# Kernel optimization log

Measured on AMD Instinct MI355X. Metric: run time of the kernel, lower is better.

Reference implementation:

```python
import jax, jax.numpy as jnp
import numpy as np

N_NODES = 100000
N_EDGES = 1600000
IN_C, HID_C, OUT_C = 128, 256, 256


def sage_conv(x, src, dst, W_l, b_l, W_r, n_nodes):
    # mean aggregation of source-node features onto destination nodes
    msg_sum = jax.ops.segment_sum(x[src], dst, num_segments=n_nodes)  # [N, F]
    deg = jax.ops.segment_sum(jnp.ones_like(dst, dtype=x.dtype), dst, num_segments=n_nodes)
    aggr = msg_sum / jnp.maximum(deg, 1.0)[:, None]
    # PyG SAGEConv: lin_l(aggr) (with bias) + lin_r(x) (no bias)
    return aggr @ W_l + b_l + x @ W_r


def setup_inputs() -> dict:
    key = jax.random.key(0)
    ks = jax.random.split(key, 12)
    x = jax.random.normal(ks[0], (N_NODES, IN_C), dtype=jnp.float32)
    edge_src = jax.random.randint(ks[1], (N_EDGES,), 0, N_NODES)
    edge_dst = jax.random.randint(ks[2], (N_EDGES,), 0, N_NODES)

    def glorot(k, fan_in, fan_out):
        s = jnp.sqrt(2.0 / (fan_in + fan_out)).astype(jnp.float32)
        return jax.random.normal(k, (fan_in, fan_out), dtype=jnp.float32) * s

    return {
        "x": x,
        "W_l0": glorot(ks[3], IN_C, HID_C), "b_l0": jnp.zeros((HID_C,), jnp.float32),
        "W_r0": glorot(ks[4], IN_C, HID_C),
        "W_l1": glorot(ks[5], HID_C, HID_C), "b_l1": jnp.zeros((HID_C,), jnp.float32),
        "W_r1": glorot(ks[6], HID_C, HID_C),
        "W_l2": glorot(ks[7], HID_C, OUT_C), "b_l2": jnp.zeros((OUT_C,), jnp.float32),
        "W_r2": glorot(ks[8], HID_C, OUT_C),
        "edge_src": edge_src,
        "edge_dst": edge_dst,
    }


def reference(x, W_l0, b_l0, W_r0, W_l1, b_l1, W_r1, W_l2, b_l2, W_r2, edge_src, edge_dst):
    n = x.shape[0]
    h = sage_conv(x, edge_src, edge_dst, W_l0, b_l0, W_r0, n)
    h = jax.nn.relu(h)  # dropout p=0.0 -> identity
    h = sage_conv(h, edge_src, edge_dst, W_l1, b_l1, W_r1, n)
    h = jax.nn.relu(h)
    h = sage_conv(h, edge_src, edge_dst, W_l2, b_l2, W_r2, n)
    return h
```

## Files before the change

kernel.cpp:

```cpp
#include <hip/hip_runtime.h>
#include <cstdint>
#include <cstddef>


#define N_NODES 100000
#define N_EDGES 1600000

#define SCAN_BLOCKS 256
#define SCAN_T 256
#define FILL_PASSES 4

typedef unsigned short ushort;
typedef unsigned int uint;
typedef __attribute__((ext_vector_type(8))) short short8;
typedef __attribute__((ext_vector_type(4))) float floatx4;

#define AS1 __attribute__((address_space(1)))
#define AS3 __attribute__((address_space(3)))

__device__ __forceinline__ float bf2f(ushort h) {
    union { uint u; float f; } c; c.u = ((uint)h) << 16; return c.f;
}
__device__ __forceinline__ ushort f2bf(float f) {
    union { float f; uint u; } c; c.f = f;
    uint u = c.u;
    return (ushort)((u + 0x7FFFu + ((u >> 16) & 1u)) >> 16);
}


#define N4X (N_NODES * 128 / 4)

__global__ void prep_all(
    const int* __restrict__ dst, int* __restrict__ cnt,
    const float* __restrict__ x, ushort* __restrict__ xb,
    const float* __restrict__ Wl0, ushort* __restrict__ Wl0t,
    const float* __restrict__ Wr0, ushort* __restrict__ Wr0t,
    const float* __restrict__ Wl1, ushort* __restrict__ Wl1t,
    const float* __restrict__ Wr1, ushort* __restrict__ Wr1t,
    const float* __restrict__ Wl2, ushort* __restrict__ Wl2t,
    const float* __restrict__ Wr2, ushort* __restrict__ Wr2t)
{
    int i = blockIdx.x * blockDim.x + threadIdx.x;
    if (i < N_EDGES) { atomicAdd(&cnt[dst[i]], 1); return; }
    i -= N_EDGES;
    if (i < N4X) {
        float4 v = *(const float4*)&x[(size_t)i * 4];
        ushort4 o;
        o.x = f2bf(v.x); o.y = f2bf(v.y); o.z = f2bf(v.z); o.w = f2bf(v.w);
        *(ushort4*)&xb[(size_t)i * 4] = o;
        return;
    }
    i -= N4X;
    if (i < 32768) { Wl0t[i] = f2bf(Wl0[(i & 127) * 256 + (i >> 7)]); return; }
    i -= 32768;
    if (i < 32768) { Wr0t[i] = f2bf(Wr0[(i & 127) * 256 + (i >> 7)]); return; }
    i -= 32768;
    if (i < 65536) { Wl1t[i] = f2bf(Wl1[(i & 255) * 256 + (i >> 8)]); return; }
    i -= 65536;
    if (i < 65536) { Wr1t[i] = f2bf(Wr1[(i & 255) * 256 + (i >> 8)]); return; }
    i -= 65536;
    if (i < 65536) { Wl2t[i] = f2bf(Wl2[(i & 255) * 256 + (i >> 8)]); return; }
    i -= 65536;
    if (i < 65536) { Wr2t[i] = f2bf(Wr2[(i & 255) * 256 + (i >> 8)]); return; }
}


__global__ __launch_bounds__(SCAN_T) void scan_partial(
    const int* __restrict__ cnt, int* __restrict__ bsum, int n)
{
    int chunk = (n + SCAN_BLOCKS - 1) / SCAN_BLOCKS;
    int beg = blockIdx.x * chunk;
    int end = beg + chunk; if (end > n) end = n;
    int t = threadIdx.x;
    int s = 0;
    for (int i = beg + t; i < end; i += SCAN_T) s += cnt[i];
    __shared__ int sh[SCAN_T];
    sh[t] = s;
    __syncthreads();
    for (int off = SCAN_T / 2; off > 0; off >>= 1) {
        if (t < off) sh[t] += sh[t + off];
        __syncthreads();
    }
    if (t == 0) bsum[blockIdx.x] = sh[0];
}

__global__ __launch_bounds__(SCAN_T) void scan_block_sums(int* __restrict__ bsum) {
    int t = threadIdx.x;
    __shared__ int sh[SCAN_T];
    int v = bsum[t];
    sh[t] = v;
    __syncthreads();
    for (int off = 1; off < SCAN_T; off <<= 1) {
        int u = (t >= off) ? sh[t - off] : 0;
        __syncthreads();
        sh[t] += u;
        __syncthreads();
    }
    bsum[t] = sh[t] - v;
}

__global__ __launch_bounds__(SCAN_T) void scan_fill(
    int* __restrict__ cnt, const int* __restrict__ bsum,
    int* __restrict__ row_ptr, int n)
{
    int chunk = (n + SCAN_BLOCKS - 1) / SCAN_BLOCKS;
    int beg = blockIdx.x * chunk;
    int end = beg + chunk; if (end > n) end = n;
    int t = threadIdx.x;
    int per = (chunk + SCAN_T - 1) / SCAN_T;
    int tb = beg + t * per;
    int te = tb + per; if (te > end) te = end;
    int s = 0;
    for (int i = tb; i < te; ++i) s += cnt[i];
    __shared__ int sh[SCAN_T];
    sh[t] = s;
    __syncthreads();
    for (int off = 1; off < SCAN_T; off <<= 1) {
        int u = (t >= off) ? sh[t - off] : 0;
        __syncthreads();
        sh[t] += u;
        __syncthreads();
    }
    int running = bsum[blockIdx.x] + sh[t] - s;
    for (int i = tb; i < te; ++i) {
        int c = cnt[i];
        row_ptr[i] = running;
        cnt[i] = running;
        running += c;
    }
    if (blockIdx.x == 0 && t == 0) row_ptr[n] = N_EDGES;
}

__global__ void fill_csr(const int* __restrict__ src, const int* __restrict__ dst,
                         int* __restrict__ cursor, int* __restrict__ col_idx) {
    int i = blockIdx.x * blockDim.x + threadIdx.x;
    if (i >= N_EDGES) return;
    int lo = (int)blockIdx.y * (N_NODES / FILL_PASSES);
    int hi = lo + (N_NODES / FILL_PASSES);
    int d = dst[i];
    if (d >= lo && d < hi) {
        int p = atomicAdd(&cursor[d], 1);
        col_idx[p] = src[i];
    }
}

__global__ __launch_bounds__(64) void aggregate_bf16(
    const ushort* __restrict__ xb, const int* __restrict__ row_ptr,
    const int* __restrict__ col_idx, ushort* __restrict__ outb, int F)
{
    int node = blockIdx.x;
    int lane = threadIdx.x;
    int half = lane >> 5, li = lane & 31;
    int b = row_ptr[node], e = row_ptr[node + 1];
    float d = (float)(e - b); if (d < 1.f) d = 1.f;
    float inv = 1.f / d;

    if (F == 256) {
        float a[8];
#pragma unroll
        for (int j = 0; j < 8; ++j) a[j] = 0.f;
        const int c = li * 8;
        int i = b;
        for (; i + 7 < e; i += 8) {
            int s0 = col_idx[i + half];
            int s1 = col_idx[i + 2 + half];
            int s2 = col_idx[i + 4 + half];
            int s3 = col_idx[i + 6 + half];
            uint4 v0 = *(const uint4*)&xb[(size_t)s0 * 256 + c];
            uint4 v1 = *(const uint4*)&xb[(size_t)s1 * 256 + c];
            uint4 v2 = *(const uint4*)&xb[(size_t)s2 * 256 + c];
            uint4 v3 = *(const uint4*)&xb[(size_t)s3 * 256 + c];
#define ACC4(v) \
            a[0] += bf2f((ushort)(v.x & 0xffff)); a[1] += bf2f((ushort)(v.x >> 16)); \
            a[2] += bf2f((ushort)(v.y & 0xffff)); a[3] += bf2f((ushort)(v.y >> 16)); \
            a[4] += bf2f((ushort)(v.z & 0xffff)); a[5] += bf2f((ushort)(v.z >> 16)); \
            a[6] += bf2f((ushort)(v.w & 0xffff)); a[7] += bf2f((ushort)(v.w >> 16));
            ACC4(v0) ACC4(v1) ACC4(v2) ACC4(v3)
        }
        for (; i + 1 < e; i += 2) {
            int s0 = col_idx[i + half];
            uint4 v0 = *(const uint4*)&xb[(size_t)s0 * 256 + c];
            ACC4(v0)
        }
        if (i < e && half == 0) {
            int s0 = col_idx[i];
            uint4 v0 = *(const uint4*)&xb[(size_t)s0 * 256 + c];
            ACC4(v0)
        }
#undef ACC4
#pragma unroll
        for (int j = 0; j < 8; ++j) a[j] += __shfl(a[j], li + 32);
        if (half == 0) {
            short8 o;
#pragma unroll
            for (int j = 0; j < 8; ++j) o[j] = (short)f2bf(a[j] * inv);
            *(short8*)&outb[(size_t)node * 256 + c] = o;
        }
    } else {
        float a[4];
#pragma unroll
        for (int j = 0; j < 4; ++j) a[j] = 0.f;
        const int c = li * 4;
        int i = b;
        for (; i + 7 < e; i += 8) {
            int s0 = col_idx[i + half];
            int s1 = col_idx[i + 2 + half];
            int s2 = col_idx[i + 4 + half];
            int s3 = col_idx[i + 6 + half];
            uint2 v0 = *(const uint2*)&xb[(size_t)s0 * 128 + c];
            uint2 v1 = *(const uint2*)&xb[(size_t)s1 * 128 + c];
            uint2 v2 = *(const uint2*)&xb[(size_t)s2 * 128 + c];
            uint2 v3 = *(const uint2*)&xb[(size_t)s3 * 128 + c];
#define ACC2(v) \
            a[0] += bf2f((ushort)(v.x & 0xffff)); a[1] += bf2f((ushort)(v.x >> 16)); \
            a[2] += bf2f((ushort)(v.y & 0xffff)); a[3] += bf2f((ushort)(v.y >> 16));
            ACC2(v0) ACC2(v1) ACC2(v2) ACC2(v3)
        }
        for (; i + 1 < e; i += 2) {
            int s0 = col_idx[i + half];
            uint2 v0 = *(const uint2*)&xb[(size_t)s0 * 128 + c];
            ACC2(v0)
        }
        if (i < e && half == 0) {
            int s0 = col_idx[i];
            uint2 v0 = *(const uint2*)&xb[(size_t)s0 * 128 + c];
            ACC2(v0)
        }
#undef ACC2
#pragma unroll
        for (int j = 0; j < 4; ++j) a[j] += __shfl(a[j], li + 32);
        if (half == 0) {
            ushort4 o;
            o.x = f2bf(a[0] * inv); o.y = f2bf(a[1] * inv);
            o.z = f2bf(a[2] * inv); o.w = f2bf(a[3] * inv);
            *(ushort4*)&outb[(size_t)node * 128 + c] = o;
        }
    }
}

__global__ __launch_bounds__(512, 1) void gemm_wres(
    const ushort* __restrict__ A1, const ushort* __restrict__ W1t,
    const ushort* __restrict__ A2, const ushort* __restrict__ W2t,
    const float* __restrict__ bias, ushort* __restrict__ out_bf,
    float* __restrict__ out_f32, int M, int K, int relu)
{
    __shared__ __align__(16) ushort Wl[32 * 256 * 8];
    int tid = threadIdx.x;
    int w = tid >> 6, lane = tid & 63;
    int m_ = lane & 15, koq = lane >> 4;
    int row0 = blockIdx.x * 256;
    int KQ = K >> 3;
    int nj = (KQ * 256) >> 9;
    int nk = K >> 5;

    floatx4 acc[2][16];
#pragma unroll
    for (int i = 0; i < 2; ++i)
#pragma unroll
        for (int f = 0; f < 16; ++f) acc[i][f] = (floatx4){0.f, 0.f, 0.f, 0.f};

    int ra = row0 + w * 32 + m_;      if (ra > M - 1) ra = M - 1;
    int rb = row0 + w * 32 + 16 + m_; if (rb > M - 1) rb = M - 1;

    for (int mm = 0; mm < 2; ++mm) {
        const ushort* __restrict__ A  = mm ? A2 : A1;
        const ushort* __restrict__ Wt = mm ? W2t : W1t;
        if (mm) __syncthreads();
        for (int j = 0; j < nj; ++j) {
            int s = j * 512 + tid;
            int q = s >> 8, col = s & 255;
            __builtin_amdgcn_global_load_lds(
                (const AS1 uint*)&Wt[(size_t)col * K + q * 8],
                (AS3 uint*)&Wl[(size_t)(j * 512 + w * 64) * 8], 16, 0, 0);
        }
        __syncthreads();

        const ushort* __restrict__ Aa = &A[(size_t)ra * K + koq * 8];
        const ushort* __restrict__ Ab = &A[(size_t)rb * K + koq * 8];

        short8 a0 = *(const short8*)&Aa[0];
        short8 a1 = *(const short8*)&Ab[0];
        for (int kk = 0; kk < nk; ++kk) {
            short8 n0, n1;
            if (kk + 1 < nk) {
                n0 = *(const short8*)&Aa[(kk + 1) * 32];
                n1 = *(const short8*)&Ab[(kk + 1) * 32];
            }
            const ushort* bbase = &Wl[(size_t)((kk * 4 + koq) * 256 + m_) * 8];
#pragma unroll
            for (int fc = 0; fc < 16; ++fc) {
                short8 b = *(const short8*)&bbase[fc * 128];
                acc[0][fc] = __builtin_amdgcn_mfma_f32_16x16x32_bf16(a0, b, acc[0][fc], 0, 0, 0);
                acc[1][fc] = __builtin_amdgcn_mfma_f32_16x16x32_bf16(a1, b, acc[1][fc], 0, 0, 0);
            }
            a0 = n0; a1 = n1;
        }
    }

#pragma unroll
    for (int m2 = 0; m2 < 2; ++m2) {
#pragma unroll
        for (int fc = 0; fc < 16; ++fc) {
            int col = fc * 16 + m_;
            float bv = bias[col];
#pragma unroll
            for (int r = 0; r < 4; ++r) {
                int row = row0 + w * 32 + m2 * 16 + koq * 4 + r;
                if (row >= M) continue;
                float v = acc[m2][fc][r] + bv;
                if (relu) v = fmaxf(v, 0.f);
                if (out_f32) out_f32[(size_t)row * 256 + col] = v;
                else         out_bf [(size_t)row * 256 + col] = f2bf(v);
            }
        }
    }
}


extern "C" void kernel_launch(void* const* d_in, const int* in_sizes, int n_in,
                              void* d_out, int out_size, void* d_ws, size_t ws_size,
                              hipStream_t stream) {
    const float* x    = (const float*)d_in[0];
    const float* W_l0 = (const float*)d_in[1];
    const float* b_l0 = (const float*)d_in[2];
    const float* W_r0 = (const float*)d_in[3];
    const float* W_l1 = (const float*)d_in[4];
    const float* b_l1 = (const float*)d_in[5];
    const float* W_r1 = (const float*)d_in[6];
    const float* W_l2 = (const float*)d_in[7];
    const float* b_l2 = (const float*)d_in[8];
    const float* W_r2 = (const float*)d_in[9];
    const int* esrc   = (const int*)d_in[10];
    const int* edst   = (const int*)d_in[11];
    float* out = (float*)d_out;

    size_t off = 0;
    char* ws = (char*)d_ws;
    auto take = [&](size_t bytes) -> void* {
        void* p = ws + off;
        off += (bytes + 255) & ~(size_t)255;
        return p;
    };
    int*    cnt     = (int*)take((size_t)N_NODES * 4);
    int*    row_ptr = (int*)take((size_t)(N_NODES + 1) * 4);
    int*    col_idx = (int*)take((size_t)N_EDGES * 4);
    int*    bsum    = (int*)take((size_t)SCAN_BLOCKS * 4);
    ushort* xb      = (ushort*)take((size_t)N_NODES * 128 * 2);
    ushort* Wl0t    = (ushort*)take((size_t)256 * 128 * 2);
    ushort* Wr0t    = (ushort*)take((size_t)256 * 128 * 2);
    ushort* Wl1t    = (ushort*)take((size_t)256 * 256 * 2);
    ushort* Wr1t    = (ushort*)take((size_t)256 * 256 * 2);
    ushort* Wl2t    = (ushort*)take((size_t)256 * 256 * 2);
    ushort* Wr2t    = (ushort*)take((size_t)256 * 256 * 2);
    ushort* aggrb   = (ushort*)take((size_t)N_NODES * 256 * 2);
    ushort* ha      = (ushort*)take((size_t)N_NODES * 256 * 2);
    ushort* hb      = (ushort*)take((size_t)N_NODES * 256 * 2);
    (void)ws_size; (void)in_sizes; (void)n_in; (void)out_size;

    hipMemsetAsync(cnt, 0, (size_t)N_NODES * 4, stream);
    int total_prep = N_EDGES + N4X + 2 * 32768 + 4 * 65536;
    prep_all<<<(total_prep + 255) / 256, 256, 0, stream>>>(
        edst, cnt, x, xb,
        W_l0, Wl0t, W_r0, Wr0t, W_l1, Wl1t, W_r1, Wr1t, W_l2, Wl2t, W_r2, Wr2t);

    scan_partial<<<SCAN_BLOCKS, SCAN_T, 0, stream>>>(cnt, bsum, N_NODES);
    scan_block_sums<<<1, SCAN_T, 0, stream>>>(bsum);
    scan_fill<<<SCAN_BLOCKS, SCAN_T, 0, stream>>>(cnt, bsum, row_ptr, N_NODES);
    int eb = (N_EDGES + 255) / 256;
    fill_csr<<<dim3(eb, FILL_PASSES), 256, 0, stream>>>(esrc, edst, cnt, col_idx);

    dim3 ggrid((N_NODES + 255) / 256, 1);

    aggregate_bf16<<<N_NODES, 64, 0, stream>>>(xb, row_ptr, col_idx, aggrb, 128);
    gemm_wres<<<ggrid, 512, 0, stream>>>(aggrb, Wl0t, xb, Wr0t, b_l0,
                                         ha, nullptr, N_NODES, 128, 1);
    aggregate_bf16<<<N_NODES, 64, 0, stream>>>(ha, row_ptr, col_idx, aggrb, 256);
    gemm_wres<<<ggrid, 512, 0, stream>>>(aggrb, Wl1t, ha, Wr1t, b_l1,
                                         hb, nullptr, N_NODES, 256, 1);
    aggregate_bf16<<<N_NODES, 64, 0, stream>>>(hb, row_ptr, col_idx, aggrb, 256);
    gemm_wres<<<ggrid, 512, 0, stream>>>(aggrb, Wl2t, hb, Wr2t, b_l2,
                                         nullptr, out, N_NODES, 256, 0);
}
```

Baseline: 837.6 us.

## Aggregate by feature slices with grid-stride node loop for cache locality

```diff
diff --git a/kernel.cpp b/kernel.cpp
--- a/kernel.cpp
+++ b/kernel.cpp
@@ -9,6 +9,8 @@
 #define SCAN_BLOCKS 256
 #define SCAN_T 256
 #define FILL_PASSES 4
+
+#define AGG_CHUNKS 2048
 
 typedef unsigned short ushort;
 typedef unsigned int uint;
@@ -144,96 +146,60 @@
     }
 }
 
-__global__ __launch_bounds__(64) void aggregate_bf16(
+__global__ __launch_bounds__(256) void aggregate_slice(
     const ushort* __restrict__ xb, const int* __restrict__ row_ptr,
     const int* __restrict__ col_idx, ushort* __restrict__ outb, int F)
 {
-    int node = blockIdx.x;
-    int lane = threadIdx.x;
-    int half = lane >> 5, li = lane & 31;
-    int b = row_ptr[node], e = row_ptr[node + 1];
-    float d = (float)(e - b); if (d < 1.f) d = 1.f;
-    float inv = 1.f / d;
-
-    if (F == 256) {
-        float a[8];
-#pragma unroll
-        for (int j = 0; j < 8; ++j) a[j] = 0.f;
-        const int c = li * 8;
+    int lane = threadIdx.x & 63;
+    int w = threadIdx.x >> 6;
+    int q = lane >> 4;
+    int j = lane & 15;
+    int nslice = (F == 256) ? 8 : 4;
+    int slice = blockIdx.x & (nslice - 1);
+    int chunk = blockIdx.x >> 3;
+    if (F == 128) chunk = blockIdx.x >> 2;
+    int c = slice * 32 + j * 2;
+    int node0 = chunk * 4 + w;
+    int nstride = AGG_CHUNKS * 4;
+
+    for (int node = node0; node < N_NODES; node += nstride) {
+        int b = row_ptr[node], e = row_ptr[node + 1];
+        float d = (float)(e - b); if (d < 1.f) d = 1.f;
+        float inv = 1.f / d;
+        float a0 = 0.f, a1 = 0.f;
         int i = b;
-        for (; i + 7 < e; i += 8) {
-            int s0 = col_idx[i + half];
-            int s1 = col_idx[i + 2 + half];
-            int s2 = col_idx[i + 4 + half];
-            int s3 = col_idx[i + 6 + half];
-            uint4 v0 = *(const uint4*)&xb[(size_t)s0 * 256 + c];
-            uint4 v1 = *(const uint4*)&xb[(size_t)s1 * 256 + c];
-            uint4 v2 = *(const uint4*)&xb[(size_t)s2 * 256 + c];
-            uint4 v3 = *(const uint4*)&xb[(size_t)s3 * 256 + c];
-#define ACC4(v) \
-            a[0] += bf2f((ushort)(v.x & 0xffff)); a[1] += bf2f((ushort)(v.x >> 16)); \
-            a[2] += bf2f((ushort)(v.y & 0xffff)); a[3] += bf2f((ushort)(v.y >> 16)); \
-            a[4] += bf2f((ushort)(v.z & 0xffff)); a[5] += bf2f((ushort)(v.z >> 16)); \
-            a[6] += bf2f((ushort)(v.w & 0xffff)); a[7] += bf2f((ushort)(v.w >> 16));
-            ACC4(v0) ACC4(v1) ACC4(v2) ACC4(v3)
-        }
-        for (; i + 1 < e; i += 2) {
-            int s0 = col_idx[i + half];
-            uint4 v0 = *(const uint4*)&xb[(size_t)s0 * 256 + c];
-            ACC4(v0)
-        }
-        if (i < e && half == 0) {
-            int s0 = col_idx[i];
-            uint4 v0 = *(const uint4*)&xb[(size_t)s0 * 256 + c];
-            ACC4(v0)
-        }
-#undef ACC4
-#pragma unroll
-        for (int j = 0; j < 8; ++j) a[j] += __shfl(a[j], li + 32);
-        if (half == 0) {
-            short8 o;
-#pragma unroll
-            for (int j = 0; j < 8; ++j) o[j] = (short)f2bf(a[j] * inv);
-            *(short8*)&outb[(size_t)node * 256 + c] = o;
-        }
-    } else {
-        float a[4];
-#pragma unroll
-        for (int j = 0; j < 4; ++j) a[j] = 0.f;
-        const int c = li * 4;
-        int i = b;
-        for (; i + 7 < e; i += 8) {
-            int s0 = col_idx[i + half];
-            int s1 = col_idx[i + 2 + half];
-            int s2 = col_idx[i + 4 + half];
-            int s3 = col_idx[i + 6 + half];
-            uint2 v0 = *(const uint2*)&xb[(size_t)s0 * 128 + c];
-            uint2 v1 = *(const uint2*)&xb[(size_t)s1 * 128 + c];
-            uint2 v2 = *(const uint2*)&xb[(size_t)s2 * 128 + c];
-            uint2 v3 = *(const uint2*)&xb[(size_t)s3 * 128 + c];
-#define ACC2(v) \
-            a[0] += bf2f((ushort)(v.x & 0xffff)); a[1] += bf2f((ushort)(v.x >> 16)); \
-            a[2] += bf2f((ushort)(v.y & 0xffff)); a[3] += bf2f((ushort)(v.y >> 16));
-            ACC2(v0) ACC2(v1) ACC2(v2) ACC2(v3)
-        }
-        for (; i + 1 < e; i += 2) {
-            int s0 = col_idx[i + half];
-            uint2 v0 = *(const uint2*)&xb[(size_t)s0 * 128 + c];
-            ACC2(v0)
-        }
-        if (i < e && half == 0) {
-            int s0 = col_idx[i];
-            uint2 v0 = *(const uint2*)&xb[(size_t)s0 * 128 + c];
-            ACC2(v0)
-        }
-#undef ACC2
-#pragma unroll
-        for (int j = 0; j < 4; ++j) a[j] += __shfl(a[j], li + 32);
-        if (half == 0) {
-            ushort4 o;
-            o.x = f2bf(a[0] * inv); o.y = f2bf(a[1] * inv);
-            o.z = f2bf(a[2] * inv); o.w = f2bf(a[3] * inv);
-            *(ushort4*)&outb[(size_t)node * 128 + c] = o;
+        for (; i + 15 < e; i += 16) {
+            int s0 = __builtin_nontemporal_load(&col_idx[i + q]);
+            int s1 = __builtin_nontemporal_load(&col_idx[i + 4 + q]);
+            int s2 = __builtin_nontemporal_load(&col_idx[i + 8 + q]);
+            int s3 = __builtin_nontemporal_load(&col_idx[i + 12 + q]);
+            uint v0 = *(const uint*)&xb[(size_t)s0 * F + c];
+            uint v1 = *(const uint*)&xb[(size_t)s1 * F + c];
+            uint v2 = *(const uint*)&xb[(size_t)s2 * F + c];
+            uint v3 = *(const uint*)&xb[(size_t)s3 * F + c];
+            a0 += bf2f((ushort)(v0 & 0xffff)); a1 += bf2f((ushort)(v0 >> 16));
+            a0 += bf2f((ushort)(v1 & 0xffff)); a1 += bf2f((ushort)(v1 >> 16));
+            a0 += bf2f((ushort)(v2 & 0xffff)); a1 += bf2f((ushort)(v2 >> 16));
+            a0 += bf2f((ushort)(v3 & 0xffff)); a1 += bf2f((ushort)(v3 >> 16));
+        }
+        for (; i + 3 < e; i += 4) {
+            int s0 = __builtin_nontemporal_load(&col_idx[i + q]);
+            uint v0 = *(const uint*)&xb[(size_t)s0 * F + c];
+            a0 += bf2f((ushort)(v0 & 0xffff)); a1 += bf2f((ushort)(v0 >> 16));
+        }
+        int rem = e - i;
+        if (q < rem) {
+            int s0 = __builtin_nontemporal_load(&col_idx[i + q]);
+            uint v0 = *(const uint*)&xb[(size_t)s0 * F + c];
+            a0 += bf2f((ushort)(v0 & 0xffff)); a1 += bf2f((ushort)(v0 >> 16));
+        }
+        a0 += __shfl_xor(a0, 16); a0 += __shfl_xor(a0, 32);
+        a1 += __shfl_xor(a1, 16); a1 += __shfl_xor(a1, 32);
+        if (q == 0) {
+            ushort2 o;
+            o.x = f2bf(a0 * inv);
+            o.y = f2bf(a1 * inv);
+            *(ushort2*)&outb[(size_t)node * F + c] = o;
         }
     }
 }
@@ -371,13 +337,13 @@
 
     dim3 ggrid((N_NODES + 255) / 256, 1);
 
-    aggregate_bf16<<<N_NODES, 64, 0, stream>>>(xb, row_ptr, col_idx, aggrb, 128);
+    aggregate_slice<<<AGG_CHUNKS * 4, 256, 0, stream>>>(xb, row_ptr, col_idx, aggrb, 128);
     gemm_wres<<<ggrid, 512, 0, stream>>>(aggrb, Wl0t, xb, Wr0t, b_l0,
                                          ha, nullptr, N_NODES, 128, 1);
-    aggregate_bf16<<<N_NODES, 64, 0, stream>>>(ha, row_ptr, col_idx, aggrb, 256);
+    aggregate_slice<<<AGG_CHUNKS * 8, 256, 0, stream>>>(ha, row_ptr, col_idx, aggrb, 256);
     gemm_wres<<<ggrid, 512, 0, stream>>>(aggrb, Wl1t, ha, Wr1t, b_l1,
                                          hb, nullptr, N_NODES, 256, 1);
-    aggregate_bf16<<<N_NODES, 64, 0, stream>>>(hb, row_ptr, col_idx, aggrb, 256);
+    aggregate_slice<<<AGG_CHUNKS * 8, 256, 0, stream>>>(hb, row_ptr, col_idx, aggrb, 256);
     gemm_wres<<<ggrid, 512, 0, stream>>>(aggrb, Wl2t, hb, Wr2t, b_l2,
                                          nullptr, out, N_NODES, 256, 0);
 }
```

Result: slower. 1.476 ms (+76.2%).

## Fuse neighbor aggregation into the SAGE GEMM via LDS-staged aggregated tile

Applied to the files above, without the earlier changes.

```diff
diff --git a/kernel.cpp b/kernel.cpp
--- a/kernel.cpp
+++ b/kernel.cpp
@@ -51,17 +51,20 @@
         return;
     }
     i -= N4X;
-    if (i < 32768) { Wl0t[i] = f2bf(Wl0[(i & 127) * 256 + (i >> 7)]); return; }
-    i -= 32768;
-    if (i < 32768) { Wr0t[i] = f2bf(Wr0[(i & 127) * 256 + (i >> 7)]); return; }
-    i -= 32768;
-    if (i < 65536) { Wl1t[i] = f2bf(Wl1[(i & 255) * 256 + (i >> 8)]); return; }
-    i -= 65536;
-    if (i < 65536) { Wr1t[i] = f2bf(Wr1[(i & 255) * 256 + (i >> 8)]); return; }
-    i -= 65536;
-    if (i < 65536) { Wl2t[i] = f2bf(Wl2[(i & 255) * 256 + (i >> 8)]); return; }
-    i -= 65536;
-    if (i < 65536) { Wr2t[i] = f2bf(Wr2[(i & 255) * 256 + (i >> 8)]); return; }
+#define WT2(Wsrc, Wdst, LIM) \
+    if (i < (LIM)) { \
+        int q = i >> 11, col = (i >> 3) & 255, e = i & 7; \
+        Wdst[i] = f2bf(Wsrc[(q * 8 + e) * 256 + col]); \
+        return; \
+    } \
+    i -= (LIM);
+    WT2(Wl0, Wl0t, 32768)
+    WT2(Wr0, Wr0t, 32768)
+    WT2(Wl1, Wl1t, 65536)
+    WT2(Wr1, Wr1t, 65536)
+    WT2(Wl2, Wl2t, 65536)
+    WT2(Wr2, Wr2t, 65536)
+#undef WT2
 }
 
 
@@ -144,174 +147,165 @@
     }
 }
 
-__global__ __launch_bounds__(64) void aggregate_bf16(
-    const ushort* __restrict__ xb, const int* __restrict__ row_ptr,
-    const int* __restrict__ col_idx, ushort* __restrict__ outb, int F)
+template <int K>
+__global__ __launch_bounds__(512, 4) void sage_fused(
+    const ushort* __restrict__ xb,
+    const int* __restrict__ row_ptr, const int* __restrict__ col_idx,
+    const ushort* __restrict__ Wlt,
+    const ushort* __restrict__ Wrt,
+    const float* __restrict__ bias,
+    ushort* __restrict__ out_bf, float* __restrict__ out_f32,
+    int M, int relu)
 {
-    int node = blockIdx.x;
-    int lane = threadIdx.x;
-    int half = lane >> 5, li = lane & 31;
-    int b = row_ptr[node], e = row_ptr[node + 1];
-    float d = (float)(e - b); if (d < 1.f) d = 1.f;
-    float inv = 1.f / d;
-
-    if (F == 256) {
-        float a[8];
-#pragma unroll
-        for (int j = 0; j < 8; ++j) a[j] = 0.f;
-        const int c = li * 8;
-        int i = b;
-        for (; i + 7 < e; i += 8) {
-            int s0 = col_idx[i + half];
-            int s1 = col_idx[i + 2 + half];
-            int s2 = col_idx[i + 4 + half];
-            int s3 = col_idx[i + 6 + half];
-            uint4 v0 = *(const uint4*)&xb[(size_t)s0 * 256 + c];
-            uint4 v1 = *(const uint4*)&xb[(size_t)s1 * 256 + c];
-            uint4 v2 = *(const uint4*)&xb[(size_t)s2 * 256 + c];
-            uint4 v3 = *(const uint4*)&xb[(size_t)s3 * 256 + c];
-#define ACC4(v) \
-            a[0] += bf2f((ushort)(v.x & 0xffff)); a[1] += bf2f((ushort)(v.x >> 16)); \
-            a[2] += bf2f((ushort)(v.y & 0xffff)); a[3] += bf2f((ushort)(v.y >> 16)); \
-            a[4] += bf2f((ushort)(v.z & 0xffff)); a[5] += bf2f((ushort)(v.z >> 16)); \
-            a[6] += bf2f((ushort)(v.w & 0xffff)); a[7] += bf2f((ushort)(v.w >> 16));
-            ACC4(v0) ACC4(v1) ACC4(v2) ACC4(v3)
-        }
-        for (; i + 1 < e; i += 2) {
-            int s0 = col_idx[i + half];
-            uint4 v0 = *(const uint4*)&xb[(size_t)s0 * 256 + c];
-            ACC4(v0)
-        }
-        if (i < e && half == 0) {
-            int s0 = col_idx[i];
-            uint4 v0 = *(const uint4*)&xb[(size_t)s0 * 256 + c];
-            ACC4(v0)
-        }
-#undef ACC4
-#pragma unroll
-        for (int j = 0; j < 8; ++j) a[j] += __shfl(a[j], li + 32);
-        if (half == 0) {
-            short8 o;
-#pragma unroll
-            for (int j = 0; j < 8; ++j) o[j] = (short)f2bf(a[j] * inv);
-            *(short8*)&outb[(size_t)node * 256 + c] = o;
-        }
-    } else {
-        float a[4];
-#pragma unroll
-        for (int j = 0; j < 4; ++j) a[j] = 0.f;
-        const int c = li * 4;
-        int i = b;
-        for (; i + 7 < e; i += 8) {
-            int s0 = col_idx[i + half];
-            int s1 = col_idx[i + 2 + half];
-            int s2 = col_idx[i + 4 + half];
-            int s3 = col_idx[i + 6 + half];
-            uint2 v0 = *(const uint2*)&xb[(size_t)s0 * 128 + c];
-            uint2 v1 = *(const uint2*)&xb[(size_t)s1 * 128 + c];
-            uint2 v2 = *(const uint2*)&xb[(size_t)s2 * 128 + c];
-            uint2 v3 = *(const uint2*)&xb[(size_t)s3 * 128 + c];
-#define ACC2(v) \
-            a[0] += bf2f((ushort)(v.x & 0xffff)); a[1] += bf2f((ushort)(v.x >> 16)); \
-            a[2] += bf2f((ushort)(v.y & 0xffff)); a[3] += bf2f((ushort)(v.y >> 16));
-            ACC2(v0) ACC2(v1) ACC2(v2) ACC2(v3)
-        }
-        for (; i + 1 < e; i += 2) {
-            int s0 = col_idx[i + half];
-            uint2 v0 = *(const uint2*)&xb[(size_t)s0 * 128 + c];
-            ACC2(v0)
-        }
-        if (i < e && half == 0) {
-            int s0 = col_idx[i];
-            uint2 v0 = *(const uint2*)&xb[(size_t)s0 * 128 + c];
-            ACC2(v0)
-        }
-#undef ACC2
-#pragma unroll
-        for (int j = 0; j < 4; ++j) a[j] += __shfl(a[j], li + 32);
-        if (half == 0) {
-            ushort4 o;
-            o.x = f2bf(a[0] * inv); o.y = f2bf(a[1] * inv);
-            o.z = f2bf(a[2] * inv); o.w = f2bf(a[3] * inv);
-            *(ushort4*)&outb[(size_t)node * 128 + c] = o;
-        }
-    }
-}
-
-__global__ __launch_bounds__(512, 1) void gemm_wres(
-    const ushort* __restrict__ A1, const ushort* __restrict__ W1t,
-    const ushort* __restrict__ A2, const ushort* __restrict__ W2t,
-    const float* __restrict__ bias, ushort* __restrict__ out_bf,
-    float* __restrict__ out_f32, int M, int K, int relu)
-{
-    __shared__ __align__(16) ushort Wl[32 * 256 * 8];
+    __shared__ __align__(16) ushort Alds[64 * 256];
+    char* lb = (char*)Alds;
     int tid = threadIdx.x;
     int w = tid >> 6, lane = tid & 63;
+    int half = lane >> 5, li = lane & 31;
+    int row0 = blockIdx.x * 64;
+
+    for (int s = 0; s < 8; ++s) {
+        int rowL = w * 8 + s;
+        int node = row0 + rowL;
+        if (node >= M) break;
+        int b = row_ptr[node], e = row_ptr[node + 1];
+        float dg = (float)(e - b); if (dg < 1.f) dg = 1.f;
+        float inv = 1.f / dg;
+        int xv = (rowL & 7) << 4;
+
+        if (K == 256) {
+            float a[8];
+#pragma unroll
+            for (int j = 0; j < 8; ++j) a[j] = 0.f;
+            const int c = li * 8;
+            int i = b;
+            for (; i + 7 < e; i += 8) {
+                int s0 = col_idx[i + half];
+                int s1 = col_idx[i + 2 + half];
+                int s2 = col_idx[i + 4 + half];
+                int s3 = col_idx[i + 6 + half];
+                uint4 v0 = *(const uint4*)&xb[(size_t)s0 * 256 + c];
+                uint4 v1 = *(const uint4*)&xb[(size_t)s1 * 256 + c];
+                uint4 v2 = *(const uint4*)&xb[(size_t)s2 * 256 + c];
+                uint4 v3 = *(const uint4*)&xb[(size_t)s3 * 256 + c];
+#define ACC4(v) \
+                a[0] += bf2f((ushort)(v.x & 0xffff)); a[1] += bf2f((ushort)(v.x >> 16)); \
+                a[2] += bf2f((ushort)(v.y & 0xffff)); a[3] += bf2f((ushort)(v.y >> 16)); \
+                a[4] += bf2f((ushort)(v.z & 0xffff)); a[5] += bf2f((ushort)(v.z >> 16)); \
+                a[6] += bf2f((ushort)(v.w & 0xffff)); a[7] += bf2f((ushort)(v.w >> 16));
+                ACC4(v0) ACC4(v1) ACC4(v2) ACC4(v3)
+            }
+            for (; i + 1 < e; i += 2) {
+                int s0 = col_idx[i + half];
+                uint4 v0 = *(const uint4*)&xb[(size_t)s0 * 256 + c];
+                ACC4(v0)
+            }
+            if (i < e && half == 0) {
+                int s0 = col_idx[i];
+                uint4 v0 = *(const uint4*)&xb[(size_t)s0 * 256 + c];
+                ACC4(v0)
+            }
+#undef ACC4
+#pragma unroll
+            for (int j = 0; j < 8; ++j) a[j] += __shfl(a[j], li + 32);
+            if (half == 0) {
+                short8 o;
+#pragma unroll
+                for (int j = 0; j < 8; ++j) o[j] = (short)f2bf(a[j] * inv);
+                int byte = (rowL * 512 + li * 16) ^ xv;
+                *(short8*)(lb + byte) = o;
+            }
+        } else {
+            float a[4];
+#pragma unroll
+            for (int j = 0; j < 4; ++j) a[j] = 0.f;
+            const int c = li * 4;
+            int i = b;
+            for (; i + 7 < e; i += 8) {
+                int s0 = col_idx[i + half];
+                int s1 = col_idx[i + 2 + half];
+                int s2 = col_idx[i + 4 + half];
+                int s3 = col_idx[i + 6 + half];
+                uint2 v0 = *(const uint2*)&xb[(size_t)s0 * 128 + c];
+                uint2 v1 = *(const uint2*)&xb[(size_t)s1 * 128 + c];
+                uint2 v2 = *(const uint2*)&xb[(size_t)s2 * 128 + c];
+                uint2 v3 = *(const uint2*)&xb[(size_t)s3 * 128 + c];
+#define ACC2(v) \
+                a[0] += bf2f((ushort)(v.x & 0xffff)); a[1] += bf2f((ushort)(v.x >> 16)); \
+                a[2] += bf2f((ushort)(v.y & 0xffff)); a[3] += bf2f((ushort)(v.y >> 16));
+                ACC2(v0) ACC2(v1) ACC2(v2) ACC2(v3)
+            }
+            for (; i + 1 < e; i += 2) {
+                int s0 = col_idx[i + half];
+                uint2 v0 = *(const uint2*)&xb[(size_t)s0 * 128 + c];
+                ACC2(v0)
+            }
+            if (i < e && half == 0) {
+                int s0 = col_idx[i];
+                uint2 v0 = *(const uint2*)&xb[(size_t)s0 * 128 + c];
+                ACC2(v0)
+            }
+#undef ACC2
+#pragma unroll
+            for (int j = 0; j < 4; ++j) a[j] += __shfl(a[j], li + 32);
+            if (half == 0) {
+                ushort4 o;
+                o.x = f2bf(a[0] * inv); o.y = f2bf(a[1] * inv);
+                o.z = f2bf(a[2] * inv); o.w = f2bf(a[3] * inv);
+                int byte = (rowL * 256 + li * 8) ^ xv;
+                *(ushort4*)(lb + byte) = o;
+            }
+        }
+    }
+    __syncthreads();
+
     int m_ = lane & 15, koq = lane >> 4;
-    int row0 = blockIdx.x * 256;
-    int KQ = K >> 3;
-    int nj = (KQ * 256) >> 9;
-    int nk = K >> 5;
-
-    floatx4 acc[2][16];
-#pragma unroll
-    for (int i = 0; i < 2; ++i)
-#pragma unroll
-        for (int f = 0; f < 16; ++f) acc[i][f] = (floatx4){0.f, 0.f, 0.f, 0.f};
-
-    int ra = row0 + w * 32 + m_;      if (ra > M - 1) ra = M - 1;
-    int rb = row0 + w * 32 + 16 + m_; if (rb > M - 1) rb = M - 1;
+    int wg = w >> 1;
+    int wc = (w & 1) * 8;
+    int rowL = wg * 16 + m_;
+    int grow = row0 + rowL; if (grow > M - 1) grow = M - 1;
+    const int nk = K >> 5;
+    int xv = (rowL & 7) << 4;
+
+    floatx4 acc[8];
+#pragma unroll
+    for (int f = 0; f < 8; ++f) acc[f] = (floatx4){0.f, 0.f, 0.f, 0.f};
 
     for (int mm = 0; mm < 2; ++mm) {
-        const ushort* __restrict__ A  = mm ? A2 : A1;
-        const ushort* __restrict__ Wt = mm ? W2t : W1t;
-        if (mm) __syncthreads();
-        for (int j = 0; j < nj; ++j) {
-            int s = j * 512 + tid;
-            int q = s >> 8, col = s & 255;
-            __builtin_amdgcn_global_load_lds(
-                (const AS1 uint*)&Wt[(size_t)col * K + q * 8],
-                (AS3 uint*)&Wl[(size_t)(j * 512 + w * 64) * 8], 16, 0, 0);
+        const ushort* __restrict__ Wt = mm ? Wrt : Wlt;
+        const ushort* __restrict__ Wb = &Wt[(size_t)((koq << 8) + wc * 16 + m_) * 8];
+        const ushort* __restrict__ Ag = &xb[(size_t)grow * K + koq * 8];
+#pragma unroll 1
+        for (int g = 0; g < nk; ++g) {
+            short8 a;
+            if (mm == 0) {
+                int byte = (rowL * (K * 2) + g * 64 + koq * 16) ^ xv;
+                a = *(const short8*)(lb + byte);
+            } else {
+                a = *(const short8*)&Ag[g * 32];
+            }
+            short8 b[8];
+#pragma unroll
+            for (int j = 0; j < 8; ++j)
+                b[j] = *(const short8*)&Wb[(size_t)g * 8192 + j * 128];
+#pragma unroll
+            for (int j = 0; j < 8; ++j)
+                acc[j] = __builtin_amdgcn_mfma_f32_16x16x32_bf16(a, b[j], acc[j], 0, 0, 0);
         }
-        __syncthreads();
-
-        const ushort* __restrict__ Aa = &A[(size_t)ra * K + koq * 8];
-        const ushort* __restrict__ Ab = &A[(size_t)rb * K + koq * 8];
-
-        short8 a0 = *(const short8*)&Aa[0];
-        short8 a1 = *(const short8*)&Ab[0];
-        for (int kk = 0; kk < nk; ++kk) {
-            short8 n0, n1;
-            if (kk + 1 < nk) {
-                n0 = *(const short8*)&Aa[(kk + 1) * 32];
-                n1 = *(const short8*)&Ab[(kk + 1) * 32];
-            }
-            const ushort* bbase = &Wl[(size_t)((kk * 4 + koq) * 256 + m_) * 8];
-#pragma unroll
-            for (int fc = 0; fc < 16; ++fc) {
-                short8 b = *(const short8*)&bbase[fc * 128];
-                acc[0][fc] = __builtin_amdgcn_mfma_f32_16x16x32_bf16(a0, b, acc[0][fc], 0, 0, 0);
-                acc[1][fc] = __builtin_amdgcn_mfma_f32_16x16x32_bf16(a1, b, acc[1][fc], 0, 0, 0);
-            }
-            a0 = n0; a1 = n1;
-        }
-    }
-
-#pragma unroll
-    for (int m2 = 0; m2 < 2; ++m2) {
-#pragma unroll
-        for (int fc = 0; fc < 16; ++fc) {
-            int col = fc * 16 + m_;
-            float bv = bias[col];
-#pragma unroll
-            for (int r = 0; r < 4; ++r) {
-                int row = row0 + w * 32 + m2 * 16 + koq * 4 + r;
-                if (row >= M) continue;
-                float v = acc[m2][fc][r] + bv;
-                if (relu) v = fmaxf(v, 0.f);
-                if (out_f32) out_f32[(size_t)row * 256 + col] = v;
-                else         out_bf [(size_t)row * 256 + col] = f2bf(v);
-            }
+    }
+
+#pragma unroll
+    for (int fc = 0; fc < 8; ++fc) {
+        int col = (wc + fc) * 16 + m_;
+        float bv = bias[col];
+#pragma unroll
+        for (int r = 0; r < 4; ++r) {
+            int row = row0 + wg * 16 + koq * 4 + r;
+            if (row >= M) continue;
+            float v = acc[fc][r] + bv;
+            if (relu) v = fmaxf(v, 0.f);
+            if (out_f32) out_f32[(size_t)row * 256 + col] = v;
+            else         out_bf [(size_t)row * 256 + col] = f2bf(v);
         }
     }
 }
@@ -352,7 +346,6 @@
     ushort* Wr1t    = (ushort*)take((size_t)256 * 256 * 2);
     ushort* Wl2t    = (ushort*)take((size_t)256 * 256 * 2);
     ushort* Wr2t    = (ushort*)take((size_t)256 * 256 * 2);
-    ushort* aggrb   = (ushort*)take((size_t)N_NODES * 256 * 2);
     ushort* ha      = (ushort*)take((size_t)N_NODES * 256 * 2);
     ushort* hb      = (ushort*)take((size_t)N_NODES * 256 * 2);
     (void)ws_size; (void)in_sizes; (void)n_in; (void)out_size;
@@ -369,15 +362,12 @@
     int eb = (N_EDGES + 255) / 256;
     fill_csr<<<dim3(eb, FILL_PASSES), 256, 0, stream>>>(esrc, edst, cnt, col_idx);
 
-    dim3 ggrid((N_NODES + 255) / 256, 1);
-
-    aggregate_bf16<<<N_NODES, 64, 0, stream>>>(xb, row_ptr, col_idx, aggrb, 128);
-    gemm_wres<<<ggrid, 512, 0, stream>>>(aggrb, Wl0t, xb, Wr0t, b_l0,
-                                         ha, nullptr, N_NODES, 128, 1);
-    aggregate_bf16<<<N_NODES, 64, 0, stream>>>(ha, row_ptr, col_idx, aggrb, 256);
-    gemm_wres<<<ggrid, 512, 0, stream>>>(aggrb, Wl1t, ha, Wr1t, b_l1,
-                                         hb, nullptr, N_NODES, 256, 1);
-    aggregate_bf16<<<N_NODES, 64, 0, stream>>>(hb, row_ptr, col_idx, aggrb, 256);
-    gemm_wres<<<ggrid, 512, 0, stream>>>(aggrb, Wl2t, hb, Wr2t, b_l2,
-                                         nullptr, out, N_NODES, 256, 0);
-}
+    int fgrid = (N_NODES + 63) / 64;
+
+    sage_fused<128><<<fgrid, 512, 0, stream>>>(
+        xb, row_ptr, col_idx, Wl0t, Wr0t, b_l0, ha, nullptr, N_NODES, 1);
+    sage_fused<256><<<fgrid, 512, 0, stream>>>(
+        ha, row_ptr, col_idx, Wl1t, Wr1t, b_l1, hb, nullptr, N_NODES, 1);
+    sage_fused<256><<<fgrid, 512, 0, stream>>>(
+        hb, row_ptr, col_idx, Wl2t, Wr2t, b_l2, nullptr, out, N_NODES, 0);
+}
```

Measured after the change: 788.2 us. 5.9% less time.
